# Kernel optimization log

Hardware: AMD Instinct MI355X
Metric: run time of the kernel (lower is better)

## Reference

```python
import jax, jax.numpy as jnp
import numpy as np

HIDDEN = 1024
HEADS = 16
HEAD = HIDDEN // HEADS
EXPAND = 4096
EPS = 1e-5


def layer_norm(x, g, b):
    mu = jnp.mean(x, axis=-1, keepdims=True)
    var = jnp.mean((x - mu) ** 2, axis=-1, keepdims=True)
    return (x - mu) * jax.lax.rsqrt(var + EPS) * g + b


def setup_inputs() -> dict:
    key = jax.random.key(0)
    ks = jax.random.split(key, 12)
    s = 0.02
    return {
        "x": jax.random.normal(ks[0], (4, 2048, HIDDEN), dtype=jnp.float32),
        "Wqkv": jax.random.normal(ks[1], (HIDDEN, 3 * HIDDEN), dtype=jnp.float32) * s,
        "bqkv": jnp.zeros((3 * HIDDEN,), jnp.float32),
        "Wproj": jax.random.normal(ks[2], (HIDDEN, HIDDEN), dtype=jnp.float32) * s,
        "bproj": jnp.zeros((HIDDEN,), jnp.float32),
        "W1": jax.random.normal(ks[3], (HIDDEN, EXPAND), dtype=jnp.float32) * s,
        "b1": jnp.zeros((EXPAND,), jnp.float32),
        "W2": jax.random.normal(ks[4], (EXPAND, HIDDEN), dtype=jnp.float32) * s,
        "b2": jnp.zeros((HIDDEN,), jnp.float32),
        "g1": jnp.ones((HIDDEN,), jnp.float32),
        "be1": jnp.zeros((HIDDEN,), jnp.float32),
        "g2": jnp.ones((HIDDEN,), jnp.float32),
        "be2": jnp.zeros((HIDDEN,), jnp.float32),
    }


def attention(x, Wqkv, bqkv, Wproj, bproj):
    B, L, _ = x.shape
    qkv = (x @ Wqkv + bqkv).reshape(B, L, 3, HEADS, HEAD)
    q, k, v = [qkv[:, :, i].transpose(0, 2, 1, 3) for i in range(3)]  # [B,H,L,D]
    attn = jnp.einsum("bnld,bnkd->bnlk", q, k) / np.sqrt(HEAD).astype(np.float32)
    attn = jax.nn.softmax(attn, axis=-1)
    o = jnp.einsum("bnlk,bnkd->bnld", attn, v)
    o = o.transpose(0, 2, 1, 3).reshape(B, L, HIDDEN)
    return o @ Wproj + bproj


def reference(x, Wqkv, bqkv, Wproj, bproj, W1, b1, W2, b2, g1, be1, g2, be2):
    # post-norm transformer block (pre_norm=False), dropout=0 (eval)
    h = layer_norm(x + attention(x, Wqkv, bqkv, Wproj, bproj), g1, be1)
    ff = jax.nn.gelu(h @ W1 + b1, approximate=False) @ W2 + b2
    return layer_norm(h + ff, g2, be2)
```

## Files before the change

### kernel.cpp

```cpp
#include <hip/hip_runtime.h>
#include <hip/hip_bf16.h>
#include <math.h>


typedef __bf16 bf16_t;
typedef __bf16 bf16x8 __attribute__((ext_vector_type(8)));
typedef __bf16 bf16x4 __attribute__((ext_vector_type(4)));
typedef float f32x4 __attribute__((ext_vector_type(4)));
typedef float f32x16 __attribute__((ext_vector_type(16)));

#define HID   1024
#define NHEAD 16
#define HD    64
#define EXPD  4096
#define LSEQ  2048
#define BATCH 4
#define MROWS (BATCH * LSEQ)

#if __has_builtin(__builtin_amdgcn_exp2f)
#define EXP2F __builtin_amdgcn_exp2f
#else
#define EXP2F exp2f
#endif

__device__ __forceinline__ void gld_lds16(const bf16_t* g, bf16_t* l) {
  __builtin_amdgcn_global_load_lds(
      (const __attribute__((address_space(1))) void*)g,
      (__attribute__((address_space(3))) void*)l, 16, 0, 0);
}

__device__ __forceinline__ void vmwait(int n) {
  if (n == 8)      asm volatile("s_waitcnt vmcnt(8)" ::: "memory");
  else if (n == 4) asm volatile("s_waitcnt vmcnt(4)" ::: "memory");
  else if (n == 3) asm volatile("s_waitcnt vmcnt(3)" ::: "memory");
  else if (n == 0) asm volatile("s_waitcnt vmcnt(0)" ::: "memory");
}

__device__ __forceinline__ void block_bar() {
  asm volatile("" ::: "memory");
  __builtin_amdgcn_s_barrier();
  asm volatile("" ::: "memory");
}

__device__ __forceinline__ void swap32(unsigned& a, unsigned& b) {
#if __has_builtin(__builtin_amdgcn_permlane32_swap)
  auto r = __builtin_amdgcn_permlane32_swap(a, b, false, false);
  a = r[0]; b = r[1];
#else
  bool hiL = ((threadIdx.x & 63) >= 32);
  unsigned pa = (unsigned)__shfl_xor((int)a, 32, 64);
  unsigned pb = (unsigned)__shfl_xor((int)b, 32, 64);
  unsigned na = hiL ? pb : a;
  unsigned nb = hiL ? b : pa;
  a = na; b = nb;
#endif
}

__device__ __forceinline__ unsigned pk_bf16(float lo, float hi) {
  bf16_t l = (bf16_t)lo, h = (bf16_t)hi;
  unsigned short ul, uh;
  __builtin_memcpy(&ul, &l, 2);
  __builtin_memcpy(&uh, &h, 2);
  return (unsigned)ul | ((unsigned)uh << 16);
}

__device__ __forceinline__ float gelu_t(float v) {
  float u = v * (0.7978845608028654f + 0.0356774081f * v * v);
  float e = EXP2F(u * 2.885390082f);
  float th = (e - 1.f) / (e + 1.f);
  return 0.5f * v * (1.f + th);
}

__global__ __launch_bounds__(256) void cvt_bf16(const float* __restrict__ in,
                                                bf16_t* __restrict__ out, int n4) {
  int i = blockIdx.x * 256 + threadIdx.x;
  if (i >= n4) return;
  float4 v = ((const float4*)in)[i];
  bf16x4 o;
  o[0] = (bf16_t)v.x; o[1] = (bf16_t)v.y; o[2] = (bf16_t)v.z; o[3] = (bf16_t)v.w;
  ((bf16x4*)out)[i] = o;
}

__global__ __launch_bounds__(256) void transpose_cvt(const float* __restrict__ W,
                                                     bf16_t* __restrict__ Wt,
                                                     int K, int N) {
  __shared__ float tile[32][33];
  int n0 = blockIdx.x * 32, k0 = blockIdx.y * 32;
  int tx = threadIdx.x & 31, ty = threadIdx.x >> 5;
#pragma unroll
  for (int i = 0; i < 32; i += 8)
    tile[ty + i][tx] = W[(size_t)(k0 + ty + i) * N + n0 + tx];
  __syncthreads();
#pragma unroll
  for (int i = 0; i < 32; i += 8)
    Wt[(size_t)(n0 + ty + i) * K + k0 + tx] = (bf16_t)tile[tx][ty + i];
}

template <int BM, int BN, int NTHR>
__global__ __launch_bounds__(NTHR, (NTHR == 512 ? 4 : 3))
void gemm_k(const bf16_t* __restrict__ A,
            const bf16_t* __restrict__ Bt,
            const float* __restrict__ bias,
            void* __restrict__ C,
            float* __restrict__ C2,
            bf16_t* __restrict__ vTo,
            int M, int N, int K, int mode) {
  constexpr int WC = (NTHR / 64) / 2;
  constexpr int AL = BM * 4 / NTHR;
  constexpr int BL = BN * 4 / NTHR;
  constexpr int LOADS = AL + BL;
  constexpr int RSTEP = NTHR >> 2;
  __shared__ bf16_t smem[3 * BM * 32 + 3 * BN * 32];
  bf16_t* As = smem;
  bf16_t* Bs = smem + 3 * BM * 32;

  const int nbx = gridDim.x;
  int p = blockIdx.y * nbx + blockIdx.x;
  const int GM = 8;
  int group = p / (GM * nbx);
  int idx = p - group * (GM * nbx);
  const int by = group * GM + (idx & (GM - 1));
  const int bx = idx >> 3;
  const int n0 = bx * BN, m0 = by * BM;

  const int zz = blockIdx.z;
  const int kLen = K / (int)gridDim.z;
  const int kOff = zz * kLen;

  const int t = threadIdx.x;
  const int lane = t & 63, w = t >> 6;
  const int wr = w / WC, wc = w % WC;
  const int quad = lane >> 4, l16 = lane & 15;

  f32x4 acc[4][4];
#pragma unroll
  for (int i = 0; i < 4; ++i)
#pragma unroll
    for (int j = 0; j < 4; ++j) acc[i][j] = (f32x4){0.f, 0.f, 0.f, 0.f};

  const int r0 = t >> 2;
  const unsigned ksw = (((unsigned)t & 3u) ^ ((unsigned)(r0 >> 1) & 3u)) * 8u;
  const unsigned offR0 = (unsigned)r0 * (unsigned)K + ksw;

  const bf16_t* aB = A + (size_t)m0 * K + kOff;
  const bf16_t* bB = Bt + (size_t)n0 * K + kOff;

  unsigned aoff[4], boff[4];
#pragma unroll
  for (int i = 0; i < 4; ++i) {
    int row = wr * 64 + 16 * i + l16;
    aoff[i] = (unsigned)(row * 32 + (quad ^ ((row >> 1) & 3)) * 8);
  }
#pragma unroll
  for (int j = 0; j < 4; ++j) {
    int row = wc * 64 + 16 * j + l16;
    boff[j] = (unsigned)(row * 32 + (quad ^ ((row >> 1) & 3)) * 8);
  }

  auto stage = [&](int slot, int kk) {
    bf16_t* Asl = As + slot * (BM * 32);
    bf16_t* Bsl = Bs + slot * (BN * 32);
    const bf16_t* aS = aB + kk;
    const bf16_t* bS = bB + kk;
#pragma unroll
    for (int a = 0; a < AL; ++a)
      gld_lds16(aS + offR0 + (size_t)a * RSTEP * K, Asl + (t + a * NTHR) * 8);
#pragma unroll
    for (int b = 0; b < BL; ++b)
      gld_lds16(bS + offR0 + (size_t)b * RSTEP * K, Bsl + (t + b * NTHR) * 8);
  };

  const int NT = kLen >> 5;

  stage(0, 0);
  stage(1, 32);
  vmwait(LOADS);
  block_bar();

  int cs = 0;
  for (int kt = 0; kt < NT; ++kt) {
    if (kt < NT - 2) {
      int ss = cs == 0 ? 2 : cs - 1;
      stage(ss, (kt + 2) * 32);
    }
    const bf16_t* Asl = As + cs * (BM * 32);
    const bf16_t* Bsl = Bs + cs * (BN * 32);
    bf16x8 af[4], bfr[4];
#pragma unroll
    for (int i = 0; i < 4; ++i) af[i] = *(const bf16x8*)(Asl + aoff[i]);
#pragma unroll
    for (int j = 0; j < 4; ++j) bfr[j] = *(const bf16x8*)(Bsl + boff[j]);
    __builtin_amdgcn_s_setprio(1);
#pragma unroll
    for (int i = 0; i < 4; ++i)
#pragma unroll
      for (int j = 0; j < 4; ++j)
        acc[i][j] = __builtin_amdgcn_mfma_f32_16x16x32_bf16(af[i], bfr[j], acc[i][j], 0, 0, 0);
    __builtin_amdgcn_s_setprio(0);
    if (kt < NT - 2)      vmwait(LOADS);
    else if (kt == NT - 2) vmwait(0);
    if (kt < NT - 1) block_bar();
    cs = cs == 2 ? 0 : cs + 1;
  }

  if constexpr (BN == 256) {
    if (vTo != nullptr && n0 >= 2048) {
      const int bb = m0 >> 11;
      const int l0b = m0 & 2047;
      block_bar();
      bf16_t* T = smem;
#pragma unroll
      for (int i = 0; i < 4; ++i) {
        int rl = wr * 64 + 16 * i + quad * 4;
#pragma unroll
        for (int j = 0; j < 4; ++j) {
          int c = wc * 64 + 16 * j + l16;
          float bv = bias[n0 + c];
          bf16x4 pk;
#pragma unroll
          for (int r = 0; r < 4; ++r) pk[r] = (bf16_t)(acc[i][j][r] + bv);
          *(bf16x4*)(T + c * 132 + rl) = pk;
        }
      }
      block_bar();
      const int vbase = n0 - 2048;
#pragma unroll
      for (int s = 0; s < 4096 / NTHR; ++s) {
        int id = t + s * NTHR;
        int c = id >> 4, ch = id & 15;
        int hh = (vbase + c) >> 6, dd = (vbase + c) & 63;
        bf16x8 v8 = *(const bf16x8*)(T + c * 132 + ch * 8);
        *(bf16x8*)(vTo + ((size_t)((bb * 16 + hh) * 64 + dd)) * 2048 + l0b + ch * 8) = v8;
      }
      return;
    }
  }

#pragma unroll
  for (int i = 0; i < 4; ++i) {
    int rowb = m0 + wr * 64 + 16 * i + quad * 4;
#pragma unroll
    for (int j = 0; j < 4; ++j) {
      int col = n0 + wc * 64 + 16 * j + l16;
      float bv = (zz == 0) ? bias[col] : 0.f;
#pragma unroll
      for (int r = 0; r < 4; ++r) {
        float v = acc[i][j][r] + bv;
        size_t idx = (size_t)(rowb + r) * N + col;
        if (zz != 0) {
          C2[idx] = v;
        } else if (mode == 0) {
          ((bf16_t*)C)[idx] = (bf16_t)v;
        } else if (mode == 1) {
          ((bf16_t*)C)[idx] = (bf16_t)gelu_t(v);
        } else {
          ((float*)C)[idx] = v;
        }
      }
    }
  }
}

__global__ __launch_bounds__(512, 2)
void gemm_8x(const bf16_t* __restrict__ A,
             const bf16_t* __restrict__ Bt,
             const float* __restrict__ bias,
             bf16_t* __restrict__ C,
             int M, int N, int K) {
  __shared__ bf16_t smem[65536];
  const int nbx = gridDim.x;
  int p = blockIdx.y * nbx + blockIdx.x;
  const int GM = 8;
  int group = p / (GM * nbx);
  int idx = p - group * (GM * nbx);
  const int by = group * GM + (idx & (GM - 1));
  const int bx = idx >> 3;
  const int n0 = bx * 256, m0 = by * 256;

  const int t = threadIdx.x;
  const int lane = t & 63, w = t >> 6;
  const int wr = w >> 2, wc = w & 3;
  const int quad = lane >> 4, l16 = lane & 15;

  f32x4 acc[8][4];
#pragma unroll
  for (int i = 0; i < 8; ++i)
#pragma unroll
    for (int j = 0; j < 4; ++j) acc[i][j] = (f32x4){0.f, 0.f, 0.f, 0.f};

  const int r0 = t >> 2;
  const unsigned ksw = (((unsigned)t & 3u) ^ ((unsigned)(r0 >> 1) & 3u)) * 8u;
  const unsigned offR = (unsigned)r0 * (unsigned)K + ksw;

  const bf16_t* aB = A + (size_t)m0 * K;
  const bf16_t* bB = Bt + (size_t)n0 * K;

  unsigned aoff[8], boff[4];
#pragma unroll
  for (int i = 0; i < 8; ++i) {
    int row = wr * 128 + 16 * i + l16;
    aoff[i] = (unsigned)(row * 32 + (quad ^ ((row >> 1) & 3)) * 8);
  }
#pragma unroll
  for (int j = 0; j < 4; ++j) {
    int row = wc * 64 + 16 * j + l16;
    boff[j] = (unsigned)(16384 + row * 32 + (quad ^ ((row >> 1) & 3)) * 8);
  }

  auto stageChunk = [&](const bf16_t* src, int kk, int regionElem) {
    bf16_t* d = smem + regionElem;
    gld_lds16(src + kk + offR, d + t * 8);
    gld_lds16(src + kk + offR + (size_t)128 * K, d + t * 8 + 4096);
  };

  const int NT = K >> 6;

  stageChunk(aB, 0, 0);
  stageChunk(bB, 0, 16384);
  stageChunk(aB, 32, 8192);
  stageChunk(bB, 32, 24576);
  vmwait(4);
  block_bar();

  for (int kt = 0; kt < NT; ++kt) {
    const int sb = (kt & 1) * 32768;
    const int ss = ((kt + 1) & 1) * 32768;
    const int ktk = (kt + 1) * 64;
    const bool st = (kt + 1 < NT);
    bf16x8 af[8], b0, b1;
#pragma unroll
    for (int i = 0; i < 8; ++i) af[i] = *(const bf16x8*)(smem + sb + aoff[i]);
    b0 = *(const bf16x8*)(smem + sb + boff[0]);
    b1 = *(const bf16x8*)(smem + sb + boff[1]);
    if (st) stageChunk(aB, ktk, ss);
    __builtin_amdgcn_s_setprio(1);
#pragma unroll
    for (int i = 0; i < 8; ++i) {
      acc[i][0] = __builtin_amdgcn_mfma_f32_16x16x32_bf16(af[i], b0, acc[i][0], 0, 0, 0);
      acc[i][1] = __builtin_amdgcn_mfma_f32_16x16x32_bf16(af[i], b1, acc[i][1], 0, 0, 0);
    }
    __builtin_amdgcn_s_setprio(0);
    b0 = *(const bf16x8*)(smem + sb + boff[2]);
    b1 = *(const bf16x8*)(smem + sb + boff[3]);
    if (st) stageChunk(bB, ktk, ss + 16384);
    __builtin_amdgcn_s_setprio(1);
#pragma unroll
    for (int i = 0; i < 8; ++i) {
      acc[i][2] = __builtin_amdgcn_mfma_f32_16x16x32_bf16(af[i], b0, acc[i][2], 0, 0, 0);
      acc[i][3] = __builtin_amdgcn_mfma_f32_16x16x32_bf16(af[i], b1, acc[i][3], 0, 0, 0);
    }
    __builtin_amdgcn_s_setprio(0);
    if (st) vmwait(4); else vmwait(0);
    block_bar();
#pragma unroll
    for (int i = 0; i < 8; ++i) af[i] = *(const bf16x8*)(smem + sb + 8192 + aoff[i]);
    b0 = *(const bf16x8*)(smem + sb + 8192 + boff[0]);
    b1 = *(const bf16x8*)(smem + sb + 8192 + boff[1]);
    if (st) stageChunk(aB, ktk + 32, ss + 8192);
    __builtin_amdgcn_s_setprio(1);
#pragma unroll
    for (int i = 0; i < 8; ++i) {
      acc[i][0] = __builtin_amdgcn_mfma_f32_16x16x32_bf16(af[i], b0, acc[i][0], 0, 0, 0);
      acc[i][1] = __builtin_amdgcn_mfma_f32_16x16x32_bf16(af[i], b1, acc[i][1], 0, 0, 0);
    }
    __builtin_amdgcn_s_setprio(0);
    b0 = *(const bf16x8*)(smem + sb + 8192 + boff[2]);
    b1 = *(const bf16x8*)(smem + sb + 8192 + boff[3]);
    if (st) stageChunk(bB, ktk + 32, ss + 24576);
    __builtin_amdgcn_s_setprio(1);
#pragma unroll
    for (int i = 0; i < 8; ++i) {
      acc[i][2] = __builtin_amdgcn_mfma_f32_16x16x32_bf16(af[i], b0, acc[i][2], 0, 0, 0);
      acc[i][3] = __builtin_amdgcn_mfma_f32_16x16x32_bf16(af[i], b1, acc[i][3], 0, 0, 0);
    }
    __builtin_amdgcn_s_setprio(0);
    if (st) {
      vmwait(4);
      block_bar();
    }
  }

#pragma unroll
  for (int i = 0; i < 8; ++i) {
    int rowb = m0 + wr * 128 + 16 * i + quad * 4;
#pragma unroll
    for (int j = 0; j < 4; ++j) {
      int col = n0 + wc * 64 + 16 * j + l16;
      float bv = bias[col];
#pragma unroll
      for (int r = 0; r < 4; ++r) {
        float v = acc[i][j][r] + bv;
        C[(size_t)(rowb + r) * N + col] = (bf16_t)gelu_t(v);
      }
    }
  }
}

__global__ __launch_bounds__(256, 2) void attn_kernel(const bf16_t* __restrict__ qkv,
                                                      const bf16_t* __restrict__ vT,
                                                      bf16_t* __restrict__ ob) {
  __shared__ bf16_t smem[32768];
  bf16_t* Qs = smem + 16384;
  const int qt = blockIdx.x, h = blockIdx.y, b = blockIdx.z;
  const int t = threadIdx.x, lane = t & 63, w = t >> 6;
  const int l32 = lane & 31, hi = lane >> 5;
  const size_t RS = 3 * HID;
  const int bh = b * NHEAD + h;

  const bf16_t* qbase = qkv + ((size_t)(b * LSEQ + qt * 256)) * RS + h * HD;
  const bf16_t* kbase = qkv + ((size_t)b * LSEQ) * RS + HID + h * HD;
  const bf16_t* vtbase = vT + (size_t)bh * HD * LSEQ;

#pragma unroll
  for (int s = 0; s < 8; ++s) {
    int l = t + s * 256;
    int r = l >> 3, c8 = l & 7;
    gld_lds16(qbase + (size_t)r * RS + ((c8 ^ (r & 7)) * 8), Qs + l * 8);
  }
  __syncthreads();

  const float sc = 0.18033688011112042f;
  bf16x8 bqA[4], bqB[4];
  {
    int qA = 64 * w + l32, qB = qA + 32;
#pragma unroll
    for (int c = 0; c < 4; ++c) {
      int y = 2 * c + hi;
      bf16x8 qa = *(const bf16x8*)(Qs + qA * 64 + ((y ^ (qA & 7)) * 8));
      bf16x8 qb = *(const bf16x8*)(Qs + qB * 64 + ((y ^ (qB & 7)) * 8));
#pragma unroll
      for (int e = 0; e < 8; ++e) {
        qa[e] = (bf16_t)((float)qa[e] * sc);
        qb[e] = (bf16_t)((float)qb[e] * sc);
      }
      bqA[c] = qa;
      bqB[c] = qb;
    }
  }

  bf16x8 ones8;
#pragma unroll
  for (int e = 0; e < 8; ++e) ones8[e] = (bf16_t)1.0f;

  auto stageKV = [&](int slot, int kt) {
    bf16_t* Ks = smem + slot * 8192;
    bf16_t* Vts = Ks + 4096;
#pragma unroll
    for (int s = 0; s < 2; ++s) {
      int l = t + s * 256;
      int r = l >> 3, c8 = l & 7;
      gld_lds16(kbase + (size_t)(kt * 64 + r) * RS + ((c8 ^ (r & 7)) * 8), Ks + l * 8);
      gld_lds16(vtbase + (size_t)r * LSEQ + kt * 64 + ((c8 ^ (r & 7)) * 8), Vts + l * 8);
    }
  };

  f32x16 accOA[2], accOB[2], accSA, accSB, z16;
#pragma unroll
  for (int e = 0; e < 16; ++e) {
    accOA[0][e] = 0.f; accOA[1][e] = 0.f;
    accOB[0][e] = 0.f; accOB[1][e] = 0.f;
    accSA[e] = 0.f; accSB[e] = 0.f; z16[e] = 0.f;
  }

  constexpr int NT = LSEQ / 64;
  stageKV(0, 0);

  for (int kt = 0; kt < NT; ++kt) {
    const int cs = kt & 1;
    if (kt + 1 < NT) {
      stageKV(1 - cs, kt + 1);
      vmwait(4);
    } else {
      vmwait(0);
    }
    block_bar();
    const bf16_t* Ks = smem + cs * 8192;
    const bf16_t* Vts = Ks + 4096;

    f32x16 sA0, sA1, sB0, sB1;
    __builtin_amdgcn_s_setprio(1);
    {
      int y = hi;
      int r0 = l32, r1 = 32 + l32;
      bf16x8 a0 = *(const bf16x8*)(Ks + r0 * 64 + ((y ^ (r0 & 7)) * 8));
      bf16x8 a1 = *(const bf16x8*)(Ks + r1 * 64 + ((y ^ (r1 & 7)) * 8));
      sA0 = __builtin_amdgcn_mfma_f32_32x32x16_bf16(a0, bqA[0], z16, 0, 0, 0);
      sA1 = __builtin_amdgcn_mfma_f32_32x32x16_bf16(a1, bqA[0], z16, 0, 0, 0);
      sB0 = __builtin_amdgcn_mfma_f32_32x32x16_bf16(a0, bqB[0], z16, 0, 0, 0);
      sB1 = __builtin_amdgcn_mfma_f32_32x32x16_bf16(a1, bqB[0], z16, 0, 0, 0);
    }
#pragma unroll
    for (int c = 1; c < 4; ++c) {
      int y = 2 * c + hi;
      int r0 = l32, r1 = 32 + l32;
      bf16x8 a0 = *(const bf16x8*)(Ks + r0 * 64 + ((y ^ (r0 & 7)) * 8));
      bf16x8 a1 = *(const bf16x8*)(Ks + r1 * 64 + ((y ^ (r1 & 7)) * 8));
      sA0 = __builtin_amdgcn_mfma_f32_32x32x16_bf16(a0, bqA[c], sA0, 0, 0, 0);
      sA1 = __builtin_amdgcn_mfma_f32_32x32x16_bf16(a1, bqA[c], sA1, 0, 0, 0);
      sB0 = __builtin_amdgcn_mfma_f32_32x32x16_bf16(a0, bqB[c], sB0, 0, 0, 0);
      sB1 = __builtin_amdgcn_mfma_f32_32x32x16_bf16(a1, bqB[c], sB1, 0, 0, 0);
    }
    __builtin_amdgcn_s_setprio(0);

    unsigned pfA[2][2][4], pfB[2][2][4];
    auto mkpf = [&](f32x16& s0, f32x16& s1, unsigned (&pf)[2][2][4]) {
#pragma unroll
      for (int stile = 0; stile < 2; ++stile) {
        f32x16& sv = stile ? s1 : s0;
        float p[16];
#pragma unroll
        for (int e = 0; e < 16; ++e) p[e] = EXP2F(sv[e]);
        unsigned lo[4], hi_[4];
#pragma unroll
        for (int g = 0; g < 4; ++g) {
          lo[g] = pk_bf16(p[4 * g + 0], p[4 * g + 1]);
          hi_[g] = pk_bf16(p[4 * g + 2], p[4 * g + 3]);
        }
#pragma unroll
        for (int c2 = 0; c2 < 2; ++c2) {
          unsigned aL = lo[2 * c2], bL = lo[2 * c2 + 1];
          swap32(aL, bL);
          pf[stile][c2][0] = aL; pf[stile][c2][2] = bL;
          unsigned aH = hi_[2 * c2], bH = hi_[2 * c2 + 1];
          swap32(aH, bH);
          pf[stile][c2][1] = aH; pf[stile][c2][3] = bH;
        }
      }
    };
    mkpf(sA0, sA1, pfA);
    mkpf(sB0, sB1, pfB);

    __builtin_amdgcn_s_setprio(1);
#pragma unroll
    for (int dt = 0; dt < 2; ++dt)
#pragma unroll
      for (int stile = 0; stile < 2; ++stile)
#pragma unroll
        for (int c2 = 0; c2 < 2; ++c2) {
          int c8v = stile * 4 + c2 * 2 + hi;
          int rv = dt * 32 + l32;
          bf16x8 av = *(const bf16x8*)(Vts + rv * 64 + ((c8v ^ (rv & 7)) * 8));
          union { unsigned u[4]; bf16x8 v; } ba, bb;
          ba.u[0] = pfA[stile][c2][0]; ba.u[1] = pfA[stile][c2][1];
          ba.u[2] = pfA[stile][c2][2]; ba.u[3] = pfA[stile][c2][3];
          bb.u[0] = pfB[stile][c2][0]; bb.u[1] = pfB[stile][c2][1];
          bb.u[2] = pfB[stile][c2][2]; bb.u[3] = pfB[stile][c2][3];
          accOA[dt] = __builtin_amdgcn_mfma_f32_32x32x16_bf16(av, ba.v, accOA[dt], 0, 0, 0);
          accOB[dt] = __builtin_amdgcn_mfma_f32_32x32x16_bf16(av, bb.v, accOB[dt], 0, 0, 0);
        }
#pragma unroll
    for (int stile = 0; stile < 2; ++stile)
#pragma unroll
      for (int c2 = 0; c2 < 2; ++c2) {
        union { unsigned u[4]; bf16x8 v; } ba, bb;
        ba.u[0] = pfA[stile][c2][0]; ba.u[1] = pfA[stile][c2][1];
        ba.u[2] = pfA[stile][c2][2]; ba.u[3] = pfA[stile][c2][3];
        bb.u[0] = pfB[stile][c2][0]; bb.u[1] = pfB[stile][c2][1];
        bb.u[2] = pfB[stile][c2][2]; bb.u[3] = pfB[stile][c2][3];
        accSA = __builtin_amdgcn_mfma_f32_32x32x16_bf16(ones8, ba.v, accSA, 0, 0, 0);
        accSB = __builtin_amdgcn_mfma_f32_32x32x16_bf16(ones8, bb.v, accSB, 0, 0, 0);
      }
    __builtin_amdgcn_s_setprio(0);
    block_bar();
  }

  float invA = 1.f / accSA[0];
  float invB = 1.f / accSB[0];

  bf16_t* Osh = smem;
  {
    int qA = 64 * w + l32, qB = qA + 32;
#pragma unroll
    for (int dt = 0; dt < 2; ++dt)
#pragma unroll
      for (int e = 0; e < 16; ++e) {
        int d = dt * 32 + (e & 3) + 8 * (e >> 2) + 4 * hi;
        Osh[qA * 68 + d] = (bf16_t)(accOA[dt][e] * invA);
        Osh[qB * 68 + d] = (bf16_t)(accOB[dt][e] * invB);
      }
  }
  __syncthreads();
#pragma unroll
  for (int s = 0; s < 8; ++s) {
    int l = t + s * 256;
    int r = l >> 3, c8 = l & 7;
    bf16x8 v = *(const bf16x8*)(Osh + r * 68 + c8 * 8);
    *(bf16x8*)(ob + ((size_t)(b * LSEQ + qt * 256 + r)) * HID + h * HD + c8 * 8) = v;
  }
}

__global__ __launch_bounds__(256) void resid_ln(const float* __restrict__ X,
                                                const float* __restrict__ Y,
                                                const float* __restrict__ Y2,
                                                const float* __restrict__ g,
                                                const float* __restrict__ be,
                                                float* __restrict__ outf,
                                                bf16_t* __restrict__ outb) {
  const int row = blockIdx.x;
  const int t = threadIdx.x;
  float4 a = ((const float4*)X)[(size_t)row * 256 + t];
  float4 bvec = ((const float4*)Y)[(size_t)row * 256 + t];
  float4 cvec = {0.f, 0.f, 0.f, 0.f};
  if (Y2) cvec = ((const float4*)Y2)[(size_t)row * 256 + t];
  float v0 = a.x + bvec.x + cvec.x, v1 = a.y + bvec.y + cvec.y;
  float v2 = a.z + bvec.z + cvec.z, v3 = a.w + bvec.w + cvec.w;
  float s = v0 + v1 + v2 + v3;
  float s2 = v0 * v0 + v1 * v1 + v2 * v2 + v3 * v3;
#pragma unroll
  for (int msk = 1; msk < 64; msk <<= 1) {
    s += __shfl_xor(s, msk, 64);
    s2 += __shfl_xor(s2, msk, 64);
  }
  __shared__ float red[8];
  int w = t >> 6;
  if ((t & 63) == 0) { red[w] = s; red[w + 4] = s2; }
  __syncthreads();
  s = red[0] + red[1] + red[2] + red[3];
  s2 = red[4] + red[5] + red[6] + red[7];
  float mu = s * (1.f / 1024.f);
  float var = s2 * (1.f / 1024.f) - mu * mu;
  float rstd = rsqrtf(var + 1e-5f);
  float4 gg = ((const float4*)g)[t];
  float4 bb = ((const float4*)be)[t];
  float o0 = (v0 - mu) * rstd * gg.x + bb.x;
  float o1 = (v1 - mu) * rstd * gg.y + bb.y;
  float o2 = (v2 - mu) * rstd * gg.z + bb.z;
  float o3 = (v3 - mu) * rstd * gg.w + bb.w;
  float4 o = {o0, o1, o2, o3};
  ((float4*)outf)[(size_t)row * 256 + t] = o;
  if (outb) {
    bf16x4 ob4;
    ob4[0] = (bf16_t)o0; ob4[1] = (bf16_t)o1; ob4[2] = (bf16_t)o2; ob4[3] = (bf16_t)o3;
    ((bf16x4*)outb)[(size_t)row * 256 + t] = ob4;
  }
}

extern "C" void kernel_launch(void* const* d_in, const int* in_sizes, int n_in,
                              void* d_out, int out_size, void* d_ws, size_t ws_size,
                              hipStream_t stream) {
  const float* x     = (const float*)d_in[0];
  const float* Wqkv  = (const float*)d_in[1];
  const float* bqkv  = (const float*)d_in[2];
  const float* Wproj = (const float*)d_in[3];
  const float* bproj = (const float*)d_in[4];
  const float* W1    = (const float*)d_in[5];
  const float* b1    = (const float*)d_in[6];
  const float* W2    = (const float*)d_in[7];
  const float* b2    = (const float*)d_in[8];
  const float* g1    = (const float*)d_in[9];
  const float* be1   = (const float*)d_in[10];
  const float* g2    = (const float*)d_in[11];
  const float* be2   = (const float*)d_in[12];
  float* out = (float*)d_out;

  char* ws = (char*)d_ws;
  bf16_t* w2T    = (bf16_t*)(ws);
  float*  h      = (float*) (ws + ((size_t)8 << 20));
  float*  a_f2   = (float*) (ws + ((size_t)40 << 20));
  bf16_t* qkv_ff = (bf16_t*)(ws + ((size_t)72 << 20));
  char*   E      = ws + ((size_t)136 << 20);
  bf16_t* wqkvT  = (bf16_t*)(E);
  bf16_t* wprojT = (bf16_t*)(E + ((size_t)6 << 20));
  bf16_t* w1T    = (bf16_t*)(E + ((size_t)8 << 20));
  char*   xb_ob  = E + ((size_t)16 << 20);
  bf16_t* hb     = (bf16_t*)(E + ((size_t)32 << 20));
  float*  f2b    = (float*)E;

  bf16_t* xb    = (bf16_t*)xb_ob;
  bf16_t* ob    = (bf16_t*)xb_ob;
  bf16_t* qkvb  = qkv_ff;
  bf16_t* ff1b  = qkv_ff;
  float*  attnf = a_f2;
  float*  ff2f  = a_f2;
  bf16_t* vTg   = hb;

  dim3 blk(256);
  dim3 blk512(512);
  transpose_cvt<<<dim3(3072 / 32, 1024 / 32), blk, 0, stream>>>(Wqkv, wqkvT, 1024, 3072);
  transpose_cvt<<<dim3(1024 / 32, 1024 / 32), blk, 0, stream>>>(Wproj, wprojT, 1024, 1024);
  transpose_cvt<<<dim3(4096 / 32, 1024 / 32), blk, 0, stream>>>(W1, w1T, 1024, 4096);
  transpose_cvt<<<dim3(1024 / 32, 4096 / 32), blk, 0, stream>>>(W2, w2T, 4096, 1024);
  cvt_bf16<<<MROWS * HID / 4 / 256, blk, 0, stream>>>(x, xb, MROWS * HID / 4);

  gemm_k<128, 256, 512><<<dim3(3072 / 256, MROWS / 128), blk512, 0, stream>>>(
      xb, wqkvT, bqkv, qkvb, nullptr, vTg, MROWS, 3072, 1024, 0);
  attn_kernel<<<dim3(LSEQ / 256, NHEAD, BATCH), blk, 0, stream>>>(qkvb, vTg, ob);
  gemm_k<128, 256, 512><<<dim3(1024 / 256, MROWS / 128, 2), blk512, 0, stream>>>(
      ob, wprojT, bproj, attnf, h, nullptr, MROWS, 1024, 1024, 2);
  resid_ln<<<MROWS, blk, 0, stream>>>(x, attnf, h, g1, be1, h, hb);
  gemm_8x<<<dim3(4096 / 256, MROWS / 256), blk512, 0, stream>>>(
      hb, w1T, b1, ff1b, MROWS, 4096, 1024);
  gemm_k<128, 256, 512><<<dim3(1024 / 256, MROWS / 128, 2), blk512, 0, stream>>>(
      ff1b, w2T, b2, ff2f, f2b, nullptr, MROWS, 1024, 4096, 2);
  resid_ln<<<MROWS, blk, 0, stream>>>(h, ff2f, f2b, g2, be2, out, (bf16_t*)nullptr);
}
```

Measured before the change: 515.2 us.

## Restructure 256x256 GEMM into 4-slot pipeline and use it for FF2 split-K

Turns the 256x256 GEMM's double-buffered 64-wide K loop into a four-slot ring of 32-wide K halves that keeps three stages of loads in flight. Each half does its 32 MFMAs in one block, with barriers before and after. Split-K over blockIdx.z and a mode-selected epilogue are added so the same kernel replaces the 128x256 gemm_k for the FF2 projection. The aim is to hide more global-load latency and give FF2 bigger tiles. In exchange there are two barriers per 32-K step instead of per 64-K step.

Result: slower. 560.0 us (+8.7%).

```diff
diff --git a/kernel.cpp b/kernel.cpp
--- a/kernel.cpp
+++ b/kernel.cpp
@@ -30,7 +30,8 @@
 }
 
 __device__ __forceinline__ void vmwait(int n) {
-  if (n == 8)      asm volatile("s_waitcnt vmcnt(8)" ::: "memory");
+  if (n == 12)     asm volatile("s_waitcnt vmcnt(12)" ::: "memory");
+  else if (n == 8) asm volatile("s_waitcnt vmcnt(8)" ::: "memory");
   else if (n == 4) asm volatile("s_waitcnt vmcnt(4)" ::: "memory");
   else if (n == 3) asm volatile("s_waitcnt vmcnt(3)" ::: "memory");
   else if (n == 0) asm volatile("s_waitcnt vmcnt(0)" ::: "memory");
@@ -262,12 +263,14 @@
 }
 
 __global__ __launch_bounds__(512, 2)
-void gemm_8x(const bf16_t* __restrict__ A,
+void gemm_d3(const bf16_t* __restrict__ A,
              const bf16_t* __restrict__ Bt,
              const float* __restrict__ bias,
-             bf16_t* __restrict__ C,
-             int M, int N, int K) {
+             void* __restrict__ C,
+             float* __restrict__ C2,
+             int M, int N, int K, int mode) {
   __shared__ bf16_t smem[65536];
+
   const int nbx = gridDim.x;
   int p = blockIdx.y * nbx + blockIdx.x;
   const int GM = 8;
@@ -277,6 +280,10 @@
   const int bx = idx >> 3;
   const int n0 = bx * 256, m0 = by * 256;
 
+  const int zz = blockIdx.z;
+  const int kLen = K / (int)gridDim.z;
+  const int kOff = zz * kLen;
+
   const int t = threadIdx.x;
   const int lane = t & 63, w = t >> 6;
   const int wr = w >> 2, wc = w & 3;
@@ -292,8 +299,8 @@
   const unsigned ksw = (((unsigned)t & 3u) ^ ((unsigned)(r0 >> 1) & 3u)) * 8u;
   const unsigned offR = (unsigned)r0 * (unsigned)K + ksw;
 
-  const bf16_t* aB = A + (size_t)m0 * K;
-  const bf16_t* bB = Bt + (size_t)n0 * K;
+  const bf16_t* aB = A + (size_t)m0 * K + kOff;
+  const bf16_t* bB = Bt + (size_t)n0 * K + kOff;
 
   unsigned aoff[8], boff[4];
 #pragma unroll
@@ -304,93 +311,76 @@
 #pragma unroll
   for (int j = 0; j < 4; ++j) {
     int row = wc * 64 + 16 * j + l16;
-    boff[j] = (unsigned)(16384 + row * 32 + (quad ^ ((row >> 1) & 3)) * 8);
-  }
-
-  auto stageChunk = [&](const bf16_t* src, int kk, int regionElem) {
-    bf16_t* d = smem + regionElem;
-    gld_lds16(src + kk + offR, d + t * 8);
-    gld_lds16(src + kk + offR + (size_t)128 * K, d + t * 8 + 4096);
+    boff[j] = (unsigned)(8192 + row * 32 + (quad ^ ((row >> 1) & 3)) * 8);
+  }
+
+  auto stageHalf = [&](int slot, int hidx) {
+    bf16_t* d = smem + slot * 16384;
+    const int kk = hidx * 32;
+    gld_lds16(aB + kk + offR, d + t * 8);
+    gld_lds16(aB + kk + offR + (size_t)128 * K, d + t * 8 + 4096);
+    gld_lds16(bB + kk + offR, d + 8192 + t * 8);
+    gld_lds16(bB + kk + offR + (size_t)128 * K, d + 8192 + t * 8 + 4096);
   };
 
-  const int NT = K >> 6;
-
-  stageChunk(aB, 0, 0);
-  stageChunk(bB, 0, 16384);
-  stageChunk(aB, 32, 8192);
-  stageChunk(bB, 32, 24576);
-  vmwait(4);
-  block_bar();
-
-  for (int kt = 0; kt < NT; ++kt) {
-    const int sb = (kt & 1) * 32768;
-    const int ss = ((kt + 1) & 1) * 32768;
-    const int ktk = (kt + 1) * 64;
-    const bool st = (kt + 1 < NT);
-    bf16x8 af[8], b0, b1;
-#pragma unroll
-    for (int i = 0; i < 8; ++i) af[i] = *(const bf16x8*)(smem + sb + aoff[i]);
-    b0 = *(const bf16x8*)(smem + sb + boff[0]);
-    b1 = *(const bf16x8*)(smem + sb + boff[1]);
-    if (st) stageChunk(aB, ktk, ss);
+  auto computeHalf = [&](int slot) {
+    const bf16_t* S = smem + slot * 16384;
+    bf16x8 af[8], b0, b1, b2, b3;
+#pragma unroll
+    for (int i = 0; i < 8; ++i) af[i] = *(const bf16x8*)(S + aoff[i]);
+    b0 = *(const bf16x8*)(S + boff[0]);
+    b1 = *(const bf16x8*)(S + boff[1]);
+    b2 = *(const bf16x8*)(S + boff[2]);
+    b3 = *(const bf16x8*)(S + boff[3]);
     __builtin_amdgcn_s_setprio(1);
 #pragma unroll
     for (int i = 0; i < 8; ++i) {
       acc[i][0] = __builtin_amdgcn_mfma_f32_16x16x32_bf16(af[i], b0, acc[i][0], 0, 0, 0);
       acc[i][1] = __builtin_amdgcn_mfma_f32_16x16x32_bf16(af[i], b1, acc[i][1], 0, 0, 0);
+      acc[i][2] = __builtin_amdgcn_mfma_f32_16x16x32_bf16(af[i], b2, acc[i][2], 0, 0, 0);
+      acc[i][3] = __builtin_amdgcn_mfma_f32_16x16x32_bf16(af[i], b3, acc[i][3], 0, 0, 0);
     }
     __builtin_amdgcn_s_setprio(0);
-    b0 = *(const bf16x8*)(smem + sb + boff[2]);
-    b1 = *(const bf16x8*)(smem + sb + boff[3]);
-    if (st) stageChunk(bB, ktk, ss + 16384);
-    __builtin_amdgcn_s_setprio(1);
-#pragma unroll
-    for (int i = 0; i < 8; ++i) {
-      acc[i][2] = __builtin_amdgcn_mfma_f32_16x16x32_bf16(af[i], b0, acc[i][2], 0, 0, 0);
-      acc[i][3] = __builtin_amdgcn_mfma_f32_16x16x32_bf16(af[i], b1, acc[i][3], 0, 0, 0);
-    }
-    __builtin_amdgcn_s_setprio(0);
-    if (st) vmwait(4); else vmwait(0);
+  };
+
+  const int NH = kLen >> 5;
+
+  stageHalf(0, 0);
+  stageHalf(1, 1);
+  stageHalf(2, 2);
+
+  int i = 0;
+  for (; i < NH - 3; ++i) {
+    stageHalf((i + 3) & 3, i + 3);
+    vmwait(12);
     block_bar();
-#pragma unroll
-    for (int i = 0; i < 8; ++i) af[i] = *(const bf16x8*)(smem + sb + 8192 + aoff[i]);
-    b0 = *(const bf16x8*)(smem + sb + 8192 + boff[0]);
-    b1 = *(const bf16x8*)(smem + sb + 8192 + boff[1]);
-    if (st) stageChunk(aB, ktk + 32, ss + 8192);
-    __builtin_amdgcn_s_setprio(1);
-#pragma unroll
-    for (int i = 0; i < 8; ++i) {
-      acc[i][0] = __builtin_amdgcn_mfma_f32_16x16x32_bf16(af[i], b0, acc[i][0], 0, 0, 0);
-      acc[i][1] = __builtin_amdgcn_mfma_f32_16x16x32_bf16(af[i], b1, acc[i][1], 0, 0, 0);
-    }
-    __builtin_amdgcn_s_setprio(0);
-    b0 = *(const bf16x8*)(smem + sb + 8192 + boff[2]);
-    b1 = *(const bf16x8*)(smem + sb + 8192 + boff[3]);
-    if (st) stageChunk(bB, ktk + 32, ss + 24576);
-    __builtin_amdgcn_s_setprio(1);
-#pragma unroll
-    for (int i = 0; i < 8; ++i) {
-      acc[i][2] = __builtin_amdgcn_mfma_f32_16x16x32_bf16(af[i], b0, acc[i][2], 0, 0, 0);
-      acc[i][3] = __builtin_amdgcn_mfma_f32_16x16x32_bf16(af[i], b1, acc[i][3], 0, 0, 0);
-    }
-    __builtin_amdgcn_s_setprio(0);
-    if (st) {
-      vmwait(4);
-      block_bar();
-    }
-  }
-
-#pragma unroll
-  for (int i = 0; i < 8; ++i) {
-    int rowb = m0 + wr * 128 + 16 * i + quad * 4;
+    computeHalf(i & 3);
+    block_bar();
+  }
+  vmwait(8);  block_bar(); computeHalf(i & 3); block_bar(); ++i;
+  vmwait(4);  block_bar(); computeHalf(i & 3); block_bar(); ++i;
+  vmwait(0);  block_bar(); computeHalf(i & 3);
+
+#pragma unroll
+  for (int i2 = 0; i2 < 8; ++i2) {
+    int rowb = m0 + wr * 128 + 16 * i2 + quad * 4;
 #pragma unroll
     for (int j = 0; j < 4; ++j) {
       int col = n0 + wc * 64 + 16 * j + l16;
-      float bv = bias[col];
+      float bv = (zz == 0) ? bias[col] : 0.f;
 #pragma unroll
       for (int r = 0; r < 4; ++r) {
-        float v = acc[i][j][r] + bv;
-        C[(size_t)(rowb + r) * N + col] = (bf16_t)gelu_t(v);
+        float v = acc[i2][j][r] + bv;
+        size_t idx = (size_t)(rowb + r) * N + col;
+        if (zz != 0) {
+          C2[idx] = v;
+        } else if (mode == 1) {
+          ((bf16_t*)C)[idx] = (bf16_t)gelu_t(v);
+        } else if (mode == 0) {
+          ((bf16_t*)C)[idx] = (bf16_t)v;
+        } else {
+          ((float*)C)[idx] = v;
+        }
       }
     }
   }
@@ -688,9 +678,9 @@
   gemm_k<128, 256, 512><<<dim3(1024 / 256, MROWS / 128, 2), blk512, 0, stream>>>(
       ob, wprojT, bproj, attnf, h, nullptr, MROWS, 1024, 1024, 2);
   resid_ln<<<MROWS, blk, 0, stream>>>(x, attnf, h, g1, be1, h, hb);
-  gemm_8x<<<dim3(4096 / 256, MROWS / 256), blk512, 0, stream>>>(
-      hb, w1T, b1, ff1b, MROWS, 4096, 1024);
-  gemm_k<128, 256, 512><<<dim3(1024 / 256, MROWS / 128, 2), blk512, 0, stream>>>(
-      ff1b, w2T, b2, ff2f, f2b, nullptr, MROWS, 1024, 4096, 2);
+  gemm_d3<<<dim3(4096 / 256, MROWS / 256), blk512, 0, stream>>>(
+      hb, w1T, b1, ff1b, nullptr, MROWS, 4096, 1024, 1);
+  gemm_d3<<<dim3(1024 / 256, MROWS / 256, 2), blk512, 0, stream>>>(
+      ff1b, w2T, b2, ff2f, f2b, MROWS, 1024, 4096, 2);
   resid_ln<<<MROWS, blk, 0, stream>>>(h, ff2f, f2b, g2, be2, out, (bf16_t*)nullptr);
 }
```
